# Kernel optimization log

Hardware: AMD Instinct MI355X
Metric: run time of the kernel (lower is better)

## Reference

```python
import jax, jax.numpy as jnp
from jax import lax
import numpy as np

BS, T, DA, DZ, K = 64, 512, 16, 32, 3


def _lstm_layer(x, Wih, Whh, bih, bhh):
    # x: [B, T, in], PyTorch LSTM gate order i,f,g,o; zero initial state
    B = x.shape[0]
    H = Whh.shape[1]
    b = bih + bhh

    def step(carry, xt):
        h, c = carry
        g = xt @ Wih.T + h @ Whh.T + b  # [B, 4H]
        i, f, gg, o = jnp.split(g, 4, axis=-1)
        c = jax.nn.sigmoid(f) * c + jax.nn.sigmoid(i) * jnp.tanh(gg)
        h = jax.nn.sigmoid(o) * jnp.tanh(c)
        return (h, c), h

    h0 = jnp.zeros((B, H), x.dtype)
    _, hs = lax.scan(step, (h0, h0), jnp.swapaxes(x, 0, 1))
    return jnp.swapaxes(hs, 0, 1)


def setup_inputs() -> dict:
    key = jax.random.key(0)
    ks = jax.random.split(key, 12)
    a = jax.random.normal(ks[0], (BS, T, DA), jnp.float32)
    # mixture dynamics / emission matrices, kept near identity for stability
    A = 0.95 * jnp.eye(DZ, dtype=jnp.float32) + 0.02 * jax.random.normal(ks[1], (K, T, DZ, DZ), jnp.float32)
    C = jnp.eye(DA, DZ, dtype=jnp.float32) + 0.05 * jax.random.normal(ks[2], (K, T, DA, DZ), jnp.float32)
    R = 0.1 * jnp.eye(DA, dtype=jnp.float32)
    Q = 0.1 * jnp.eye(DZ, dtype=jnp.float32)
    mu0 = jnp.zeros((DZ,), jnp.float32)
    sigma0 = jnp.eye(DZ, dtype=jnp.float32)
    H4 = 4 * K  # LSTM hidden size = K
    Wih0 = 0.1 * jax.random.normal(ks[3], (H4, DA), jnp.float32)
    Whh0 = 0.1 * jax.random.normal(ks[4], (H4, K), jnp.float32)
    bih0 = 0.1 * jax.random.normal(ks[5], (H4,), jnp.float32)
    bhh0 = 0.1 * jax.random.normal(ks[6], (H4,), jnp.float32)
    Wih1 = 0.1 * jax.random.normal(ks[7], (H4, K), jnp.float32)
    Whh1 = 0.1 * jax.random.normal(ks[8], (H4, K), jnp.float32)
    bih1 = 0.1 * jax.random.normal(ks[9], (H4,), jnp.float32)
    bhh1 = 0.1 * jax.random.normal(ks[10], (H4,), jnp.float32)
    return {"a": a, "A": A, "C": C, "R": R, "Q": Q, "mu0": mu0, "sigma0": sigma0,
            "Wih0": Wih0, "Whh0": Whh0, "bih0": bih0, "bhh0": bhh0,
            "Wih1": Wih1, "Whh1": Whh1, "bih1": bih1, "bhh1": bhh1}


def reference(a, A, C, R, Q, mu0, sigma0, Wih0, Whh0, bih0, bhh0, Wih1, Whh1, bih1, bhh1):
    bs, T, da = a.shape
    dz = A.shape[-1]
    # dynamics network: 2-layer LSTM + softmax mixture weights alpha [bs,T,K]
    h = _lstm_layer(a, Wih0, Whh0, bih0, bhh0)
    h = _lstm_layer(h, Wih1, Whh1, bih1, bhh1)
    alpha = jax.nn.softmax(h, axis=-1)
    # mix per-mode matrices; time-major [T,bs,.,.]
    At = jnp.einsum('btk,ktij->tbij', alpha, A)
    Ct = jnp.einsum('btk,ktij->tbij', alpha, C)
    a_tm = jnp.swapaxes(a, 0, 1)  # [T,bs,da]
    I = jnp.eye(dz, dtype=a.dtype)
    mu_f0 = jnp.broadcast_to(mu0, (bs, dz))
    sig_f0 = jnp.broadcast_to(sigma0, (bs, dz, dz))

    def fstep(carry, inp):
        mu_f, mu_p, sig_p = carry  # prev filtered mean, predicted mean/cov
        a_t, A_t, C_t = inp
        # NOTE: residual uses previous *filtered* mean, matching the source code
        r = a_t - jnp.einsum('bij,bj->bi', C_t, mu_f)
        Ct_T = jnp.swapaxes(C_t, -1, -2)
        S = C_t @ sig_p @ Ct_T + R
        Kg = sig_p @ Ct_T @ jnp.linalg.inv(S)
        mu_new = mu_p + jnp.einsum('bij,bj->bi', Kg, r)
        sig_new = (I - Kg @ C_t) @ sig_p
        mu_p_new = jnp.einsum('bij,bj->bi', A_t, mu_new)
        sig_p_new = A_t @ sig_new @ jnp.swapaxes(A_t, -1, -2) + Q
        return (mu_new, mu_p_new, sig_p_new), (mu_new, sig_new, mu_p_new, sig_p_new)

    _, (mu_f, sig_f, mu_p, sig_p) = lax.scan(
        fstep, (mu_f0, mu_f0, sig_f0), (a_tm, At, Ct))

    # RTS smoothing (backward recursion), faithful to smooth()
    def sstep(carry, inp):
        mu_n, sig_n = carry
        mu_ft, sig_ft, mu_pt, sig_pt, A_next = inp
        J = sig_ft @ jnp.swapaxes(A_next, -1, -2) @ jnp.linalg.inv(sig_pt)
        mu_s = mu_ft + jnp.einsum('bij,bj->bi', J, mu_n - mu_pt)
        sig_s = sig_ft + J @ (sig_n - sig_pt)
        return (mu_s, sig_s), (mu_s, sig_s)

    _, (mu_s_rest, sig_s_rest) = lax.scan(
        sstep, (mu_f[-1], sig_f[-1]),
        (mu_f[:-1], sig_f[:-1], mu_p[:-1], sig_p[:-1], At[1:]),
        reverse=True)
    mu_s = jnp.concatenate([mu_s_rest, mu_f[-1:]], axis=0)   # [T,bs,dz]
    sig_s = jnp.concatenate([sig_s_rest, sig_f[-1:]], axis=0)  # [T,bs,dz,dz]
    out = jnp.concatenate([mu_s, sig_s.reshape(T, bs, dz * dz)], axis=-1)
    return jnp.swapaxes(out, 0, 1)  # [bs, T, dz + dz*dz]
```

## Files before the change

kernel.cpp:

```cpp
#include <hip/hip_runtime.h>
#include <hip/hip_bf16.h>

#define BSZ 64
#define TT  512
#define DA  16
#define DZ  32
#define NG  12
#define NT  256

typedef __hip_bfloat16 bf;

#define FP32_R0 0x3DCCCCCDu

__device__ __forceinline__ int mode_(const void* Rm){
  return (((const unsigned*)Rm)[0] == FP32_R0) ? 0 : 1;
}
__device__ __forceinline__ float LD(const void* p, size_t i, int b16){
  return b16 ? __bfloat162float(((const bf*)p)[i]) : ((const float*)p)[i];
}
__device__ __forceinline__ void STO(void* p, size_t i, float v, int b16){
  if (b16) ((bf*)p)[i] = __float2bfloat16(v);
  else     ((float*)p)[i] = v;
}
__device__ __forceinline__ float osan_(double vd, float code){
  float v = (float)vd;
  unsigned u = __float_as_uint(v);
  if ((u & 0x7f800000u) == 0x7f800000u)
    return ((u & 0x007fffffu) != 0u) ? code : ((u >> 31) ? -(code-1000.0f) : (code-1000.0f));
  return v;
}
__device__ __forceinline__ float sigm_(float x){ return 1.0f/(1.0f + __expf(-x)); }
__device__ __forceinline__ float tanh_(float x){ return 1.0f - 2.0f/(__expf(2.0f*x)+1.0f); }

__device__ void alpha_stage_(int b, int tid, int b16,
  const void* a, const void* Wih0, const void* bih0, const void* bhh0,
  const void* Whh0, const void* Wih1, const void* Whh1,
  const void* bih1, const void* bhh1,
  float* sxw, float* salp)
{
  for (int e=tid; e<TT*NG; e+=NT){
    int t=e/NG, g=e-NG*t;
    float s = LD(bih0,g,b16) + LD(bhh0,g,b16);
    size_t ab = ((size_t)b*TT + t)*DA;
    #pragma unroll
    for (int j=0;j<DA;++j) s += LD(Wih0,g*DA+j,b16)*LD(a,ab+j,b16);
    sxw[e] = s;
  }
  __syncthreads();
  if (tid==0){
    float w0[NG][3], wi1[NG][3], w1[NG][3], bb[NG];
    #pragma unroll
    for (int g=0;g<NG;++g){
      #pragma unroll
      for (int j=0;j<3;++j){ w0[g][j]=LD(Whh0,(size_t)g*3+j,b16); wi1[g][j]=LD(Wih1,(size_t)g*3+j,b16); w1[g][j]=LD(Whh1,(size_t)g*3+j,b16); }
      bb[g] = LD(bih1,g,b16) + LD(bhh1,g,b16);
    }
    float h1[3]={0,0,0}, c1[3]={0,0,0}, h2[3]={0,0,0}, c2[3]={0,0,0};
    for (int t=0;t<TT;++t){
      const float* xr = sxw + t*NG;
      float g1[NG];
      #pragma unroll
      for (int g=0;g<NG;++g) g1[g] = xr[g] + w0[g][0]*h1[0]+w0[g][1]*h1[1]+w0[g][2]*h1[2];
      #pragma unroll
      for (int j=0;j<3;++j){
        float iv=sigm_(g1[j]), fv=sigm_(g1[3+j]), gv=tanh_(g1[6+j]), ov=sigm_(g1[9+j]);
        c1[j] = fv*c1[j] + iv*gv;
        h1[j] = ov*tanh_(c1[j]);
      }
      float g2[NG];
      #pragma unroll
      for (int g=0;g<NG;++g) g2[g] = bb[g] + wi1[g][0]*h1[0]+wi1[g][1]*h1[1]+wi1[g][2]*h1[2]
                                            + w1[g][0]*h2[0]+w1[g][1]*h2[1]+w1[g][2]*h2[2];
      #pragma unroll
      for (int j=0;j<3;++j){
        float iv=sigm_(g2[j]), fv=sigm_(g2[3+j]), gv=tanh_(g2[6+j]), ov=sigm_(g2[9+j]);
        c2[j] = fv*c2[j] + iv*gv;
        h2[j] = ov*tanh_(c2[j]);
      }
      float m = fmaxf(h2[0], fmaxf(h2[1], h2[2]));
      float e0=__expf(h2[0]-m), e1=__expf(h2[1]-m), e2=__expf(h2[2]-m);
      float inv = 1.0f/(e0+e1+e2);
      salp[t*3+0]=e0*inv; salp[t*3+1]=e1*inv; salp[t*3+2]=e2*inv;
    }
  }
  __syncthreads();
}

__global__ __launch_bounds__(256) void k_alpha(
  const void* __restrict__ a, const void* __restrict__ Rm,
  const void* __restrict__ Wih0, const void* __restrict__ Whh0,
  const void* __restrict__ bih0, const void* __restrict__ bhh0,
  const void* __restrict__ Wih1, const void* __restrict__ Whh1,
  const void* __restrict__ bih1, const void* __restrict__ bhh1,
  float* __restrict__ alws)
{
  const int b16 = mode_(Rm);
  const int b = blockIdx.x, tid = threadIdx.x;
  __shared__ float sxw[TT*NG];
  __shared__ float salp[TT*3];
  alpha_stage_(b, tid, b16, a, Wih0, bih0, bhh0, Whh0, Wih1, Whh1, bih1, bhh1,
               sxw, salp);
  for (int e=tid;e<TT*3;e+=NT) alws[(size_t)b*TT*3+e] = salp[e];
}

__global__ __launch_bounds__(256) void k_fwd(
  const void* __restrict__ a, const void* __restrict__ Am,
  const void* __restrict__ Cm, const void* __restrict__ Rm,
  const void* __restrict__ Qm, const void* __restrict__ mu0,
  const void* __restrict__ sig0,
  const void* __restrict__ Wih0, const void* __restrict__ Whh0,
  const void* __restrict__ bih0, const void* __restrict__ bhh0,
  const void* __restrict__ Wih1, const void* __restrict__ Whh1,
  const void* __restrict__ bih1, const void* __restrict__ bhh1,
  const float* __restrict__ alws,
  void* __restrict__ out)
{
  const int b16 = mode_(Rm);
  const int b = blockIdx.x, tid = threadIdx.x;
  __shared__ double dpool[4240];
  __shared__ float sAt[1056], sCt[528], sQ[1056], sR[272], sPCt[544], sKg[544];
  __shared__ float salp[TT*3];
  __shared__ double dMu[32], dMup[32], dr[16];
  double* dPp  = dpool;
  double* dPf  = dpool+1056;
  double* dCP  = dpool+2112;
  double* dT1  = dpool+2640;
  double* dAugS= dpool+3696;
  double* dMinv= dpool+3968;

  if (alws){
    for (int e=tid;e<TT*3;e+=NT) salp[e] = alws[(size_t)b*TT*3+e];
    __syncthreads();
  } else {
    alpha_stage_(b, tid, b16, a, Wih0, bih0, bhh0, Whh0, Wih1, Whh1, bih1, bhh1,
                 (float*)dpool, salp);
  }

  for (int e=tid;e<1024;e+=NT){ int i=e>>5,j=e&31;
    sQ[i*33+j]  = LD(Qm,e,b16);
    dPp[i*33+j] = (double)LD(sig0,e,b16); }
  for (int e=tid;e<256;e+=NT){ int i=e>>4,j=e&15; sR[i*17+j] = LD(Rm,e,b16); }
  if (tid<32){ double m = (double)LD(mu0,tid,b16); dMu[tid]=m; dMup[tid]=m; }
  __syncthreads();

  const int i0 = tid>>5, j0 = tid&31;
  const int i4 = tid>>4, j4 = tid&15;

  float pA0[4],pA1[4],pA2[4],pC0[2],pC1[2],pC2[2];
  {
    size_t o0=0, o1=(size_t)TT*1024, o2=(size_t)2*TT*1024;
    #pragma unroll
    for (int q=0;q<4;++q){ int e=tid+q*NT; pA0[q]=LD(Am,o0+e,b16); pA1[q]=LD(Am,o1+e,b16); pA2[q]=LD(Am,o2+e,b16); }
    size_t c0=0, c1=(size_t)TT*512, c2=(size_t)2*TT*512;
    #pragma unroll
    for (int q=0;q<2;++q){ int e=tid+q*NT; pC0[q]=LD(Cm,c0+e,b16); pC1[q]=LD(Cm,c1+e,b16); pC2[q]=LD(Cm,c2+e,b16); }
  }

  for (int t=0;t<TT;++t){
    const size_t ob = ((size_t)b*TT+t)*1056;
    {
      float a0=salp[t*3+0], a1=salp[t*3+1], a2=salp[t*3+2];
      #pragma unroll
      for (int q=0;q<4;++q){ int e=tid+q*NT; int i=e>>5,j=e&31;
        sAt[i*33+j] = a0*pA0[q]+a1*pA1[q]+a2*pA2[q]; }
      #pragma unroll
      for (int q=0;q<2;++q){ int e=tid+q*NT; int i=e>>5,j=e&31;
        sCt[i*33+j] = a0*pC0[q]+a1*pC1[q]+a2*pC2[q]; }
    }
    if (t+1<TT){
      size_t o0=(size_t)(t+1)*1024, o1=(size_t)(TT+t+1)*1024, o2=(size_t)(2*TT+t+1)*1024;
      #pragma unroll
      for (int q=0;q<4;++q){ int e=tid+q*NT; pA0[q]=LD(Am,o0+e,b16); pA1[q]=LD(Am,o1+e,b16); pA2[q]=LD(Am,o2+e,b16); }
      size_t c0=(size_t)(t+1)*512, c1=(size_t)(TT+t+1)*512, c2=(size_t)(2*TT+t+1)*512;
      #pragma unroll
      for (int q=0;q<2;++q){ int e=tid+q*NT; pC0[q]=LD(Cm,c0+e,b16); pC1[q]=LD(Cm,c1+e,b16); pC2[q]=LD(Cm,c2+e,b16); }
    }
    __syncthreads();

    {
      double A0=0.0, A1=0.0;
      for (int k=0;k<32;++k){ double bv=dPp[k*33+j0];
        A0 += (double)sCt[i0*33+k]*bv;
        A1 += (double)sCt[(i0+8)*33+k]*bv; }
      dCP[i0*33+j0]=A0; dCP[(i0+8)*33+j0]=A1;
    }
    {
      double A0=0.0, A1=0.0;
      for (int m=0;m<32;++m){ double cv=(double)sCt[j4*33+m];
        A0 += dPp[i4*33+m]*cv;
        A1 += dPp[(i4+16)*33+m]*cv; }
      sPCt[i4*17+j4]=(float)A0; sPCt[(i4+16)*17+j4]=(float)A1;
    }
    if (tid<16){ double s = (double)LD(a,((size_t)b*TT+t)*DA+tid,b16);
      for (int k=0;k<32;++k) s -= (double)sCt[tid*33+k]*dMu[k];
      dr[tid]=s; }
    __syncthreads();

    { int i=tid>>4, j=tid&15; double v=(double)sR[i*17+j];
      for (int k=0;k<32;++k) v += dCP[i*33+k]*(double)sCt[j*33+k];
      dAugS[i*17+j]=v; }
    __syncthreads();

    if (tid < 64){
      const int r = tid>>2, q = tid&3, cbase = q*8;
      double Rg[8];
      #pragma unroll
      for (int u=0;u<8;++u){
        int c = cbase+u;
        Rg[u] = (c<16) ? dAugS[r*17+c] : ((c-16)==r ? 1.0 : 0.0);
      }
      #pragma unroll
      for (int kp=0;kp<16;++kp){
        double pv = __shfl(Rg[kp&7], (kp<<2)|(kp>>3), 64);
        if (!(fabs(pv)>1e-300)) pv=1.0;
        double ip = 1.0/pv;
        if (r==kp){
          #pragma unroll
          for (int u=0;u<8;++u){ int c=cbase+u; if (c>kp) Rg[u]*=ip; }
        }
        double rf = __shfl(Rg[kp&7], (tid&0x3C)|(kp>>3), 64);
        #pragma unroll
        for (int u=0;u<8;++u){
          double pr = __shfl(Rg[u], (kp<<2)|q, 64);
          int c=cbase+u;
          if (r!=kp && c>kp) Rg[u] -= rf*pr;
        }
      }
      if (q>=2){
        #pragma unroll
        for (int u=0;u<8;++u){ int k=cbase+u-16; dMinv[r*17+k]=Rg[u]; }
      }
    }
    __syncthreads();

    {
      double A0=0.0, A1=0.0;
      for (int l=0;l<16;++l){ double mv=dMinv[l*17+j4];
        A0 += (double)sPCt[i4*17+l]*mv;
        A1 += (double)sPCt[(i4+16)*17+l]*mv; }
      sKg[i4*17+j4]=(float)A0; sKg[(i4+16)*17+j4]=(float)A1;
    }
    __syncthreads();

    if (tid<32){ double s=dMup[tid];
      for (int k=0;k<16;++k) s += (double)sKg[tid*17+k]*dr[k];
      dMu[tid]=s;
      STO(out, ob+tid, osan_(s,5300.0f), b16);
    }
    {
      double A0=dPp[i0*33+j0], A1=dPp[(i0+8)*33+j0],
             A2=dPp[(i0+16)*33+j0], A3=dPp[(i0+24)*33+j0];
      for (int l=0;l<16;++l){ double cv=dCP[l*33+j0];
        A0 -= (double)sKg[i0*17+l]*cv;
        A1 -= (double)sKg[(i0+8)*17+l]*cv;
        A2 -= (double)sKg[(i0+16)*17+l]*cv;
        A3 -= (double)sKg[(i0+24)*17+l]*cv; }
      dPf[i0*33+j0]=A0; dPf[(i0+8)*33+j0]=A1;
      dPf[(i0+16)*33+j0]=A2; dPf[(i0+24)*33+j0]=A3;
      STO(out, ob+32+((size_t)i0<<5)+j0,      osan_(A0,5300.0f), b16);
      STO(out, ob+32+((size_t)(i0+8)<<5)+j0,  osan_(A1,5300.0f), b16);
      STO(out, ob+32+((size_t)(i0+16)<<5)+j0, osan_(A2,5300.0f), b16);
      STO(out, ob+32+((size_t)(i0+24)<<5)+j0, osan_(A3,5300.0f), b16);
    }
    __syncthreads();

    {
      double A0=0.0,A1=0.0,A2=0.0,A3=0.0;
      for (int k=0;k<32;++k){ double bv=dPf[k*33+j0];
        A0 += (double)sAt[i0*33+k]*bv;
        A1 += (double)sAt[(i0+8)*33+k]*bv;
        A2 += (double)sAt[(i0+16)*33+k]*bv;
        A3 += (double)sAt[(i0+24)*33+k]*bv; }
      dT1[i0*33+j0]=A0; dT1[(i0+8)*33+j0]=A1;
      dT1[(i0+16)*33+j0]=A2; dT1[(i0+24)*33+j0]=A3;
    }
    if (tid<32){ double s=0.0;
      for (int k=0;k<32;++k) s += (double)sAt[tid*33+k]*dMu[k];
      dMup[tid]=s; }
    __syncthreads();

    {
      double A0=(double)sQ[i0*33+j0], A1=(double)sQ[(i0+8)*33+j0],
             A2=(double)sQ[(i0+16)*33+j0], A3=(double)sQ[(i0+24)*33+j0];
      for (int k=0;k<32;++k){ double av=(double)sAt[j0*33+k];
        A0 += dT1[i0*33+k]*av;
        A1 += dT1[(i0+8)*33+k]*av;
        A2 += dT1[(i0+16)*33+k]*av;
        A3 += dT1[(i0+24)*33+k]*av; }
      dPp[i0*33+j0]=A0; dPp[(i0+8)*33+j0]=A1;
      dPp[(i0+16)*33+j0]=A2; dPp[(i0+24)*33+j0]=A3;
    }
    __syncthreads();
  }
}

__global__ __launch_bounds__(256) void k_pre(
  const void* __restrict__ Am, const void* __restrict__ Qm,
  const void* __restrict__ Rm, const void* __restrict__ outv,
  const float* __restrict__ alws, float* __restrict__ rec, int t0)
{
  const int b16 = mode_(Rm);
  const int t = t0 + blockIdx.x;
  const int b = blockIdx.y;
  const int tid = threadIdx.x;
  __shared__ double dAug[2080];
  __shared__ double dmp[32];
  __shared__ float sAtc[1056], sAtn[1056], sSf[1056], sT[1056], sF[1056], sPp[1056], sJ[1056], sQ[1056];
  __shared__ float smu[32];

  size_t obase = (size_t)b*TT*1056;
  const float* al = alws + (size_t)b*TT*3;
  float c0=al[t*3+0],     c1=al[t*3+1],     c2=al[t*3+2];
  float n0=al[(t+1)*3+0], n1=al[(t+1)*3+1], n2=al[(t+1)*3+2];
  size_t oA0c=(size_t)t*1024, oA1c=(size_t)(TT+t)*1024, oA2c=(size_t)(2*TT+t)*1024;
  size_t oA0n=oA0c+1024, oA1n=oA1c+1024, oA2n=oA2c+1024;

  for (int e=tid;e<1024;e+=NT){ int i=e>>5,j=e&31;
    sAtc[i*33+j] = c0*LD(Am,oA0c+e,b16)+c1*LD(Am,oA1c+e,b16)+c2*LD(Am,oA2c+e,b16);
    sAtn[i*33+j] = n0*LD(Am,oA0n+e,b16)+n1*LD(Am,oA1n+e,b16)+n2*LD(Am,oA2n+e,b16);
    sSf[i*33+j]  = LD(outv, obase + (size_t)t*1056 + 32 + e, b16);
    sQ[i*33+j]   = LD(Qm,e,b16);
  }
  if (tid<32) smu[tid] = LD(outv, obase + (size_t)t*1056 + tid, b16);
  __syncthreads();

  for (int e=tid;e<1024;e+=NT){ int i=e>>5, j=e&31;
    double acc=0.0, accF=0.0;
    for (int k=0;k<32;++k){
      acc  += (double)sAtc[i*33+k]*(double)sSf[k*33+j];
      accF += (double)sSf[i*33+k]*(double)sAtn[j*33+k];
    }
    sT[i*33+j]=(float)acc; sF[i*33+j]=(float)accF; }
  if (tid<32){ double s=0.0;
    for (int k=0;k<32;++k) s += (double)sAtc[tid*33+k]*(double)smu[k];
    dmp[tid]=s; }
  __syncthreads();

  for (int e=tid;e<1024;e+=NT){ int i=e>>5, j=e&31;
    double acc=(double)sQ[i*33+j];
    for (int k=0;k<32;++k) acc += (double)sT[i*33+k]*(double)sAtc[j*33+k];
    sPp[i*33+j]=(float)acc;
    dAug[i*65+j]=acc;
    dAug[i*65+32+j]=(i==j)?1.0:0.0; }
  __syncthreads();

  for (int kp=0;kp<32;++kp){
    double pv = dAug[kp*65+kp];
    if (!(fabs(pv)>1e-300)) pv=1.0;
    double ip = 1.0/pv;
    if (tid<64 && tid>kp) dAug[kp*65+tid] *= ip;
    __syncthreads();
    for (int e=tid;e<2048;e+=NT){ int i=e>>6, j=e&63;
      if (i!=kp && j>kp) dAug[i*65+j] -= dAug[i*65+kp]*dAug[kp*65+j];
    }
    __syncthreads();
  }

  float* rp = rec + ((size_t)b*gridDim.x + (size_t)blockIdx.x)*2080;

  for (int e=tid;e<1024;e+=NT){ int i=e>>5, j=e&31; double acc=0.0;
    for (int k=0;k<32;++k) acc += (double)sF[i*33+k]*dAug[k*65+32+j];
    float jv=(float)acc; sJ[i*33+j]=jv; rp[e]=jv; }
  __syncthreads();

  for (int e=tid;e<1024;e+=NT){ int i=e>>5, j=e&31;
    double acc=(double)sSf[i*33+j];
    for (int k=0;k<32;++k) acc -= (double)sJ[i*33+k]*(double)sPp[k*33+j];
    rp[1024+e]=(float)acc; }
  if (tid<32){ double acc=(double)smu[tid];
    for (int k=0;k<32;++k) acc -= (double)sJ[tid*33+k]*dmp[k];
    rp[2048+tid]=(float)acc; }
}

__global__ __launch_bounds__(256) void k_bwd(
  const void* __restrict__ Rm, void* __restrict__ outv,
  const float* __restrict__ rec, float* __restrict__ cont,
  int t0, int t1)
{
  const int b16 = mode_(Rm);
  const int b = blockIdx.x, tid = threadIdx.x;
  const int chlen = t1 - t0;
  __shared__ float sX[2][1056];
  __shared__ float sR[2080];
  size_t obase = (size_t)b*TT*1056;
  int cur = 0;
  const int i0 = tid>>5, j0 = tid&31;

  if (t1 == TT-1){
    for (int e=tid;e<1024;e+=NT){ int i=e>>5,j=e&31;
      sX[0][i*33+j] = LD(outv, obase+(size_t)(TT-1)*1056+32+e, b16); }
    if (tid<32) sX[0][tid*33+32] = LD(outv, obase+(size_t)(TT-1)*1056+tid, b16);
  } else {
    for (int e=tid;e<1056;e+=NT) sX[0][e] = cont[(size_t)b*1056+e];
  }
  float rg[9];
  {
    const float* rp = rec + ((size_t)b*chlen + (size_t)(chlen-1))*2080;
    #pragma unroll
    for (int q=0;q<9;++q){ int e=tid+q*NT; rg[q] = (e<2080)? rp[e] : 0.0f; }
  }
  __syncthreads();

  for (int t=t1-1; t>=t0; --t){
    #pragma unroll
    for (int q=0;q<9;++q){ int e=tid+q*NT; if (e<2080) sR[e]=rg[q]; }
    if (t>t0){
      const float* rp = rec + ((size_t)b*chlen + (size_t)(t-1-t0))*2080;
      #pragma unroll
      for (int q=0;q<9;++q){ int e=tid+q*NT; rg[q] = (e<2080)? rp[e] : 0.0f; }
    }
    __syncthreads();

    const float* Xc = sX[cur]; float* Xn = sX[cur^1];
    {
      double A0=(double)sR[1024+(i0<<5)+j0];
      double A1=(double)sR[1024+((i0+8)<<5)+j0];
      double A2=(double)sR[1024+((i0+16)<<5)+j0];
      double A3=(double)sR[1024+((i0+24)<<5)+j0];
      for (int k=0;k<32;++k){ double xv=(double)Xc[k*33+j0];
        A0 += (double)sR[(i0<<5)+k]*xv;
        A1 += (double)sR[((i0+8)<<5)+k]*xv;
        A2 += (double)sR[((i0+16)<<5)+k]*xv;
        A3 += (double)sR[((i0+24)<<5)+k]*xv; }
      Xn[i0*33+j0]=(float)A0;      Xn[(i0+8)*33+j0]=(float)A1;
      Xn[(i0+16)*33+j0]=(float)A2; Xn[(i0+24)*33+j0]=(float)A3;
      size_t tb = obase+(size_t)t*1056+32;
      STO(outv, tb+((size_t)i0<<5)+j0,      osan_(A0,5700.0f), b16);
      STO(outv, tb+((size_t)(i0+8)<<5)+j0,  osan_(A1,5700.0f), b16);
      STO(outv, tb+((size_t)(i0+16)<<5)+j0, osan_(A2,5700.0f), b16);
      STO(outv, tb+((size_t)(i0+24)<<5)+j0, osan_(A3,5700.0f), b16);
    }
    if (tid<32){
      double acc=(double)sR[2048+tid];
      for (int k=0;k<32;++k) acc += (double)sR[(tid<<5)+k]*(double)Xc[k*33+32];
      Xn[tid*33+32]=(float)acc;
      STO(outv, obase+(size_t)t*1056+tid, osan_(acc,5700.0f), b16);
    }
    __syncthreads();
    cur ^= 1;
  }
  for (int e=tid;e<1056;e+=NT) cont[(size_t)b*1056+e] = sX[cur][e];
}

__global__ __launch_bounds__(256) void k_smooth(
  const void* __restrict__ a, const void* __restrict__ Am,
  const void* __restrict__ Rm, const void* __restrict__ Qm,
  const void* __restrict__ Wih0, const void* __restrict__ Whh0,
  const void* __restrict__ bih0, const void* __restrict__ bhh0,
  const void* __restrict__ Wih1, const void* __restrict__ Whh1,
  const void* __restrict__ bih1, const void* __restrict__ bhh1,
  void* __restrict__ out)
{
  const int b16 = mode_(Rm);
  const int b = blockIdx.x, tid = threadIdx.x;
  __shared__ double dAug[2080];
  __shared__ float fp2[9504];
  __shared__ float salp[TT*3];
  __shared__ double dMun[32], dmp[32], sdm[32];
  float* sAtn = fp2;
  float* sAtc = fp2+1056;
  float* sSf  = fp2+2112;
  float* sSn  = fp2+3168;
  float* sT   = fp2+4224;
  float* sQ   = fp2+5280;
  float* sF   = fp2+6336;
  float* sPp32= fp2+7392;
  float* sJ   = fp2+8448;

  alpha_stage_(b, tid, b16, a, Wih0, bih0, bhh0, Whh0, Wih1, Whh1, bih1, bhh1,
               fp2, salp);

  size_t obase = (size_t)b*TT*1056;
  for (int e=tid;e<1024;e+=NT){ int i=e>>5,j=e&31;
    sQ[i*33+j]  = LD(Qm,e,b16);
    sSn[i*33+j] = LD(out, obase + (size_t)(TT-1)*1056 + 32 + e, b16); }
  if (tid<32) dMun[tid] = (double)LD(out, obase + (size_t)(TT-1)*1056 + tid, b16);
  __syncthreads();

  for (int t=TT-2; t>=0; --t){
    float n0=salp[(t+1)*3+0], n1=salp[(t+1)*3+1], n2=salp[(t+1)*3+2];
    float c0=salp[t*3+0],     c1=salp[t*3+1],     c2=salp[t*3+2];
    size_t oA0n=(size_t)(t+1)*1024, oA1n=(size_t)(TT+t+1)*1024, oA2n=(size_t)(2*TT+t+1)*1024;
    size_t oA0c=(size_t)t*1024,     oA1c=(size_t)(TT+t)*1024,   oA2c=(size_t)(2*TT+t)*1024;
    for (int e=tid;e<1024;e+=NT){ int i=e>>5,j=e&31;
      sAtn[i*33+j] = n0*LD(Am,oA0n+e,b16)+n1*LD(Am,oA1n+e,b16)+n2*LD(Am,oA2n+e,b16);
      sAtc[i*33+j] = c0*LD(Am,oA0c+e,b16)+c1*LD(Am,oA1c+e,b16)+c2*LD(Am,oA2c+e,b16);
      sSf[i*33+j]  = LD(out, obase + (size_t)t*1056 + 32 + e, b16); }
    __syncthreads();

    for (int e=tid;e<1024;e+=NT){ int i=e>>5, j=e&31;
      double acc=0.0, accF=0.0;
      for (int k=0;k<32;++k){
        acc  += (double)sAtc[i*33+k]*(double)sSf[k*33+j];
        accF += (double)sSf[i*33+k]*(double)sAtn[j*33+k];
      }
      sT[i*33+j]=(float)acc; sF[i*33+j]=(float)accF; }
    if (tid<32){ double s=0.0; float muf = LD(out, obase+(size_t)t*1056+tid, b16);
      for (int k=0;k<32;++k) s += (double)sAtc[tid*33+k]*(double)LD(out, obase+(size_t)t*1056+k, b16);
      dmp[tid]=s; (void)muf; }
    __syncthreads();

    for (int e=tid;e<1024;e+=NT){ int i=e>>5, j=e&31;
      double acc=(double)sQ[i*33+j];
      for (int k=0;k<32;++k) acc += (double)sT[i*33+k]*(double)sAtc[j*33+k];
      sPp32[i*33+j]=(float)acc;
      dAug[i*65+j]=acc;
      dAug[i*65+32+j]=(i==j)?1.0:0.0; }
    if (tid<32) sdm[tid] = dMun[tid] - dmp[tid];
    __syncthreads();

    for (int kp=0;kp<32;++kp){
      double pv = dAug[kp*65+kp];
      if (!(fabs(pv)>1e-300)) pv=1.0;
      double ip = 1.0/pv;
      if (tid<64 && tid>kp) dAug[kp*65+tid] *= ip;
      __syncthreads();
      for (int e=tid;e<2048;e+=NT){ int i=e>>6, j=e&63;
        if (i!=kp && j>kp) dAug[i*65+j] -= dAug[i*65+kp]*dAug[kp*65+j];
      }
      __syncthreads();
    }

    for (int e=tid;e<1024;e+=NT){ int i=e>>5, j=e&31; double acc=0.0;
      for (int k=0;k<32;++k) acc += (double)sF[i*33+k]*dAug[k*65+32+j];
      sJ[i*33+j]=(float)acc; }
    __syncthreads();

    if (tid<32){ double s2=0.0;
      for (int k=0;k<32;++k) s2 += (double)sJ[tid*33+k]*sdm[k];
      double v = (double)LD(out, obase+(size_t)t*1056+tid, b16) + s2;
      STO(out, obase+(size_t)t*1056+tid, osan_(v,5700.0f), b16);
      dMun[tid] = v;
    }
    float resv[4];
    { int i0 = tid>>5, j = tid&31;
      for (int s=0;s<4;++s){ int i=i0+(s<<3); double acc=0.0;
        for (int k=0;k<32;++k) acc += (double)sJ[i*33+k]*((double)sSn[k*33+j]-(double)sPp32[k*33+j]);
        double res = (double)sSf[i*33+j] + acc;
        STO(out, obase+(size_t)t*1056+32+(i<<5)+j, osan_(res,5700.0f), b16);
        resv[s]=(float)res;
      }
    }
    __syncthreads();
    { int i0 = tid>>5, j = tid&31;
      for (int s=0;s<4;++s){ int i=i0+(s<<3); sSn[i*33+j]=resv[s]; } }
    __syncthreads();
  }
}

__global__ __launch_bounds__(256) void k_fill(float* o, int n, float v){
  int i = blockIdx.x*256 + threadIdx.x;
  if (i<n) o[i]=v;
}

extern "C" void kernel_launch(void* const* d_in, const int* in_sizes, int n_in,
                              void* d_out, int out_size, void* d_ws, size_t ws_size,
                              hipStream_t stream)
{
  static const int EXP[15] = {524288,1572864,786432,256,1024,32,1024,192,36,12,12,36,36,12,12};
  int ok = (n_in==15) && (out_size==34603008);
  if (ok) for (int i=0;i<15;++i) if (in_sizes[i]!=EXP[i]) ok=0;
  if (!ok){
    k_fill<<<dim3((out_size+255)/256), dim3(256), 0, stream>>>((float*)d_out, out_size, 777.0f);
    return;
  }
  const void* a=d_in[0]; const void* Am=d_in[1]; const void* Cm=d_in[2];
  const void* Rm=d_in[3]; const void* Qm=d_in[4]; const void* mu0=d_in[5];
  const void* sig0=d_in[6];
  const void* Wih0=d_in[7]; const void* Whh0=d_in[8]; const void* bih0=d_in[9];
  const void* bhh0=d_in[10]; const void* Wih1=d_in[11]; const void* Whh1=d_in[12];
  const void* bih1=d_in[13]; const void* bhh1=d_in[14];

  const long long FIXED_F = 98304LL + 67584LL;
  long long availB = (long long)ws_size;
  int CH = 0;
  if (d_ws && availB > FIXED_F*4){
    long long ch = (availB - FIXED_F*4) / (64LL*2080LL*4LL);
    CH = (int)((ch > 511) ? 511 : ch);
  }

  if (CH >= 4){
    float* wsf  = (float*)d_ws;
    float* alws = wsf;
    float* cont = wsf + 98304;
    float* rec  = wsf + 165888;

    k_alpha<<<dim3(BSZ), dim3(NT), 0, stream>>>(a, Rm,
        Wih0, Whh0, bih0, bhh0, Wih1, Whh1, bih1, bhh1, alws);
    k_fwd  <<<dim3(BSZ), dim3(NT), 0, stream>>>(a, Am, Cm, Rm, Qm, mu0, sig0,
        Wih0, Whh0, bih0, bhh0, Wih1, Whh1, bih1, bhh1, alws, d_out);

    int t1 = TT-1;
    while (t1 > 0){
      int t0 = t1 - CH; if (t0 < 0) t0 = 0;
      int len = t1 - t0;
      k_pre<<<dim3(len, BSZ), dim3(NT), 0, stream>>>(Am, Qm, Rm, d_out, alws, rec, t0);
      k_bwd<<<dim3(BSZ), dim3(NT), 0, stream>>>(Rm, d_out, rec, cont, t0, t1);
      t1 = t0;
    }
  } else {
    k_fwd   <<<dim3(BSZ), dim3(NT), 0, stream>>>(a, Am, Cm, Rm, Qm, mu0, sig0,
               Wih0, Whh0, bih0, bhh0, Wih1, Whh1, bih1, bhh1, (const float*)nullptr, d_out);
    k_smooth<<<dim3(BSZ), dim3(NT), 0, stream>>>(a, Am, Rm, Qm,
               Wih0, Whh0, bih0, bhh0, Wih1, Whh1, bih1, bhh1, d_out);
  }
}
```

Before: 10.67 ms.

## Cache forward predicted covariances in workspace for the smoother precompute

The forward filter now writes each step's predicted mean and covariance to workspace. The smoother precompute kernel reads them back instead of recomputing A_t·Σ·A_tᵀ+Q and A_t·μ, which removes two 32x32 double matmuls per timestep. The cost is a 128MB workspace buffer and extra global writes in the serial forward kernel, plus smaller chunks for the backward pass if workspace is tight. Many inner loops also get unroll pragmas, and one Xc column is hoisted into registers in the backward kernel.

```diff
diff --git a/kernel.cpp b/kernel.cpp
--- a/kernel.cpp
+++ b/kernel.cpp
@@ -32,13 +32,13 @@
 __device__ __forceinline__ float sigm_(float x){ return 1.0f/(1.0f + __expf(-x)); }
 __device__ __forceinline__ float tanh_(float x){ return 1.0f - 2.0f/(__expf(2.0f*x)+1.0f); }
 
-__device__ void alpha_stage_(int b, int tid, int b16,
+__device__ void alpha_stage_(int b, int tid, int nt, int b16,
   const void* a, const void* Wih0, const void* bih0, const void* bhh0,
   const void* Whh0, const void* Wih1, const void* Whh1,
   const void* bih1, const void* bhh1,
   float* sxw, float* salp)
 {
-  for (int e=tid; e<TT*NG; e+=NT){
+  for (int e=tid; e<TT*NG; e+=nt){
     int t=e/NG, g=e-NG*t;
     float s = LD(bih0,g,b16) + LD(bhh0,g,b16);
     size_t ab = ((size_t)b*TT + t)*DA;
@@ -98,7 +98,7 @@
   const int b = blockIdx.x, tid = threadIdx.x;
   __shared__ float sxw[TT*NG];
   __shared__ float salp[TT*3];
-  alpha_stage_(b, tid, b16, a, Wih0, bih0, bhh0, Whh0, Wih1, Whh1, bih1, bhh1,
+  alpha_stage_(b, tid, NT, b16, a, Wih0, bih0, bhh0, Whh0, Wih1, Whh1, bih1, bhh1,
                sxw, salp);
   for (int e=tid;e<TT*3;e+=NT) alws[(size_t)b*TT*3+e] = salp[e];
 }
@@ -113,6 +113,7 @@
   const void* __restrict__ Wih1, const void* __restrict__ Whh1,
   const void* __restrict__ bih1, const void* __restrict__ bhh1,
   const float* __restrict__ alws,
+  float* __restrict__ psig, float* __restrict__ pmu,
   void* __restrict__ out)
 {
   const int b16 = mode_(Rm);
@@ -132,7 +133,7 @@
     for (int e=tid;e<TT*3;e+=NT) salp[e] = alws[(size_t)b*TT*3+e];
     __syncthreads();
   } else {
-    alpha_stage_(b, tid, b16, a, Wih0, bih0, bhh0, Whh0, Wih1, Whh1, bih1, bhh1,
+    alpha_stage_(b, tid, NT, b16, a, Wih0, bih0, bhh0, Whh0, Wih1, Whh1, bih1, bhh1,
                  (float*)dpool, salp);
   }
 
@@ -276,7 +277,9 @@
     }
     if (tid<32){ double s=0.0;
       for (int k=0;k<32;++k) s += (double)sAt[tid*33+k]*dMu[k];
-      dMup[tid]=s; }
+      dMup[tid]=s;
+      if (pmu) pmu[((size_t)b*TT+t)*32+tid] = (float)s;
+    }
     __syncthreads();
 
     {
@@ -289,6 +292,13 @@
         A3 += dT1[(i0+24)*33+k]*av; }
       dPp[i0*33+j0]=A0; dPp[(i0+8)*33+j0]=A1;
       dPp[(i0+16)*33+j0]=A2; dPp[(i0+24)*33+j0]=A3;
+      if (psig){
+        size_t pb = ((size_t)b*TT+t)*1024;
+        psig[pb+((size_t)i0<<5)+j0]      = (float)A0;
+        psig[pb+((size_t)(i0+8)<<5)+j0]  = (float)A1;
+        psig[pb+((size_t)(i0+16)<<5)+j0] = (float)A2;
+        psig[pb+((size_t)(i0+24)<<5)+j0] = (float)A3;
+      }
     }
     __syncthreads();
   }
@@ -297,7 +307,9 @@
 __global__ __launch_bounds__(256) void k_pre(
   const void* __restrict__ Am, const void* __restrict__ Qm,
   const void* __restrict__ Rm, const void* __restrict__ outv,
-  const float* __restrict__ alws, float* __restrict__ rec, int t0)
+  const float* __restrict__ alws,
+  const float* __restrict__ psig, const float* __restrict__ pmu,
+  float* __restrict__ rec, int t0)
 {
   const int b16 = mode_(Rm);
   const int t = t0 + blockIdx.x;
@@ -310,39 +322,67 @@
 
   size_t obase = (size_t)b*TT*1056;
   const float* al = alws + (size_t)b*TT*3;
-  float c0=al[t*3+0],     c1=al[t*3+1],     c2=al[t*3+2];
   float n0=al[(t+1)*3+0], n1=al[(t+1)*3+1], n2=al[(t+1)*3+2];
-  size_t oA0c=(size_t)t*1024, oA1c=(size_t)(TT+t)*1024, oA2c=(size_t)(2*TT+t)*1024;
-  size_t oA0n=oA0c+1024, oA1n=oA1c+1024, oA2n=oA2c+1024;
-
-  for (int e=tid;e<1024;e+=NT){ int i=e>>5,j=e&31;
-    sAtc[i*33+j] = c0*LD(Am,oA0c+e,b16)+c1*LD(Am,oA1c+e,b16)+c2*LD(Am,oA2c+e,b16);
-    sAtn[i*33+j] = n0*LD(Am,oA0n+e,b16)+n1*LD(Am,oA1n+e,b16)+n2*LD(Am,oA2n+e,b16);
-    sSf[i*33+j]  = LD(outv, obase + (size_t)t*1056 + 32 + e, b16);
-    sQ[i*33+j]   = LD(Qm,e,b16);
-  }
-  if (tid<32) smu[tid] = LD(outv, obase + (size_t)t*1056 + tid, b16);
-  __syncthreads();
-
-  for (int e=tid;e<1024;e+=NT){ int i=e>>5, j=e&31;
-    double acc=0.0, accF=0.0;
-    for (int k=0;k<32;++k){
-      acc  += (double)sAtc[i*33+k]*(double)sSf[k*33+j];
-      accF += (double)sSf[i*33+k]*(double)sAtn[j*33+k];
-    }
-    sT[i*33+j]=(float)acc; sF[i*33+j]=(float)accF; }
-  if (tid<32){ double s=0.0;
-    for (int k=0;k<32;++k) s += (double)sAtc[tid*33+k]*(double)smu[k];
-    dmp[tid]=s; }
-  __syncthreads();
-
-  for (int e=tid;e<1024;e+=NT){ int i=e>>5, j=e&31;
-    double acc=(double)sQ[i*33+j];
-    for (int k=0;k<32;++k) acc += (double)sT[i*33+k]*(double)sAtc[j*33+k];
-    sPp[i*33+j]=(float)acc;
-    dAug[i*65+j]=acc;
-    dAug[i*65+32+j]=(i==j)?1.0:0.0; }
-  __syncthreads();
+  size_t oA0n=(size_t)(t+1)*1024, oA1n=(size_t)(TT+t+1)*1024, oA2n=(size_t)(2*TT+t+1)*1024;
+
+  if (psig){
+    const float* pb = psig + ((size_t)b*TT+t)*1024;
+    for (int e=tid;e<1024;e+=NT){ int i=e>>5,j=e&31;
+      sAtn[i*33+j] = n0*LD(Am,oA0n+e,b16)+n1*LD(Am,oA1n+e,b16)+n2*LD(Am,oA2n+e,b16);
+      sSf[i*33+j]  = LD(outv, obase + (size_t)t*1056 + 32 + e, b16);
+      float sp = pb[e];
+      sPp[i*33+j] = sp;
+      dAug[i*65+j] = (double)sp;
+      dAug[i*65+32+j] = (i==j)?1.0:0.0;
+    }
+    if (tid<32){
+      smu[tid] = LD(outv, obase + (size_t)t*1056 + tid, b16);
+      dmp[tid] = (double)pmu[((size_t)b*TT+t)*32+tid];
+    }
+    __syncthreads();
+
+    for (int e=tid;e<1024;e+=NT){ int i=e>>5, j=e&31;
+      double accF=0.0;
+      #pragma unroll
+      for (int k=0;k<32;++k) accF += (double)sSf[i*33+k]*(double)sAtn[j*33+k];
+      sF[i*33+j]=(float)accF; }
+    __syncthreads();
+  } else {
+    float c0=al[t*3+0], c1=al[t*3+1], c2=al[t*3+2];
+    size_t oA0c=(size_t)t*1024, oA1c=(size_t)(TT+t)*1024, oA2c=(size_t)(2*TT+t)*1024;
+
+    for (int e=tid;e<1024;e+=NT){ int i=e>>5,j=e&31;
+      sAtc[i*33+j] = c0*LD(Am,oA0c+e,b16)+c1*LD(Am,oA1c+e,b16)+c2*LD(Am,oA2c+e,b16);
+      sAtn[i*33+j] = n0*LD(Am,oA0n+e,b16)+n1*LD(Am,oA1n+e,b16)+n2*LD(Am,oA2n+e,b16);
+      sSf[i*33+j]  = LD(outv, obase + (size_t)t*1056 + 32 + e, b16);
+      sQ[i*33+j]   = LD(Qm,e,b16);
+    }
+    if (tid<32) smu[tid] = LD(outv, obase + (size_t)t*1056 + tid, b16);
+    __syncthreads();
+
+    for (int e=tid;e<1024;e+=NT){ int i=e>>5, j=e&31;
+      double acc=0.0, accF=0.0;
+      #pragma unroll
+      for (int k=0;k<32;++k){
+        acc  += (double)sAtc[i*33+k]*(double)sSf[k*33+j];
+        accF += (double)sSf[i*33+k]*(double)sAtn[j*33+k];
+      }
+      sT[i*33+j]=(float)acc; sF[i*33+j]=(float)accF; }
+    if (tid<32){ double s=0.0;
+      #pragma unroll
+      for (int k=0;k<32;++k) s += (double)sAtc[tid*33+k]*(double)smu[k];
+      dmp[tid]=s; }
+    __syncthreads();
+
+    for (int e=tid;e<1024;e+=NT){ int i=e>>5, j=e&31;
+      double acc=(double)sQ[i*33+j];
+      #pragma unroll
+      for (int k=0;k<32;++k) acc += (double)sT[i*33+k]*(double)sAtc[j*33+k];
+      sPp[i*33+j]=(float)acc;
+      dAug[i*65+j]=acc;
+      dAug[i*65+32+j]=(i==j)?1.0:0.0; }
+    __syncthreads();
+  }
 
   for (int kp=0;kp<32;++kp){
     double pv = dAug[kp*65+kp];
@@ -350,7 +390,8 @@
     double ip = 1.0/pv;
     if (tid<64 && tid>kp) dAug[kp*65+tid] *= ip;
     __syncthreads();
-    for (int e=tid;e<2048;e+=NT){ int i=e>>6, j=e&63;
+    #pragma unroll
+    for (int q=0;q<8;++q){ int e=tid+q*NT; int i=e>>6, j=e&63;
       if (i!=kp && j>kp) dAug[i*65+j] -= dAug[i*65+kp]*dAug[kp*65+j];
     }
     __syncthreads();
@@ -359,15 +400,18 @@
   float* rp = rec + ((size_t)b*gridDim.x + (size_t)blockIdx.x)*2080;
 
   for (int e=tid;e<1024;e+=NT){ int i=e>>5, j=e&31; double acc=0.0;
+    #pragma unroll
     for (int k=0;k<32;++k) acc += (double)sF[i*33+k]*dAug[k*65+32+j];
     float jv=(float)acc; sJ[i*33+j]=jv; rp[e]=jv; }
   __syncthreads();
 
   for (int e=tid;e<1024;e+=NT){ int i=e>>5, j=e&31;
     double acc=(double)sSf[i*33+j];
+    #pragma unroll
     for (int k=0;k<32;++k) acc -= (double)sJ[i*33+k]*(double)sPp[k*33+j];
     rp[1024+e]=(float)acc; }
   if (tid<32){ double acc=(double)smu[tid];
+    #pragma unroll
     for (int k=0;k<32;++k) acc -= (double)sJ[tid*33+k]*dmp[k];
     rp[2048+tid]=(float)acc; }
 }
@@ -413,11 +457,15 @@
 
     const float* Xc = sX[cur]; float* Xn = sX[cur^1];
     {
+      float colX[32];
+      #pragma unroll
+      for (int k=0;k<32;++k) colX[k] = Xc[k*33+j0];
       double A0=(double)sR[1024+(i0<<5)+j0];
       double A1=(double)sR[1024+((i0+8)<<5)+j0];
       double A2=(double)sR[1024+((i0+16)<<5)+j0];
       double A3=(double)sR[1024+((i0+24)<<5)+j0];
-      for (int k=0;k<32;++k){ double xv=(double)Xc[k*33+j0];
+      #pragma unroll
+      for (int k=0;k<32;++k){ double xv=(double)colX[k];
         A0 += (double)sR[(i0<<5)+k]*xv;
         A1 += (double)sR[((i0+8)<<5)+k]*xv;
         A2 += (double)sR[((i0+16)<<5)+k]*xv;
@@ -432,6 +480,7 @@
     }
     if (tid<32){
       double acc=(double)sR[2048+tid];
+      #pragma unroll
       for (int k=0;k<32;++k) acc += (double)sR[(tid<<5)+k]*(double)Xc[k*33+32];
       Xn[tid*33+32]=(float)acc;
       STO(outv, obase+(size_t)t*1056+tid, osan_(acc,5700.0f), b16);
@@ -467,7 +516,7 @@
   float* sPp32= fp2+7392;
   float* sJ   = fp2+8448;
 
-  alpha_stage_(b, tid, b16, a, Wih0, bih0, bhh0, Whh0, Wih1, Whh1, bih1, bhh1,
+  alpha_stage_(b, tid, NT, b16, a, Wih0, bih0, bhh0, Whh0, Wih1, Whh1, bih1, bhh1,
                fp2, salp);
 
   size_t obase = (size_t)b*TT*1056;
@@ -490,18 +539,21 @@
 
     for (int e=tid;e<1024;e+=NT){ int i=e>>5, j=e&31;
       double acc=0.0, accF=0.0;
+      #pragma unroll
       for (int k=0;k<32;++k){
         acc  += (double)sAtc[i*33+k]*(double)sSf[k*33+j];
         accF += (double)sSf[i*33+k]*(double)sAtn[j*33+k];
       }
       sT[i*33+j]=(float)acc; sF[i*33+j]=(float)accF; }
     if (tid<32){ double s=0.0; float muf = LD(out, obase+(size_t)t*1056+tid, b16);
+      #pragma unroll
       for (int k=0;k<32;++k) s += (double)sAtc[tid*33+k]*(double)LD(out, obase+(size_t)t*1056+k, b16);
       dmp[tid]=s; (void)muf; }
     __syncthreads();
 
     for (int e=tid;e<1024;e+=NT){ int i=e>>5, j=e&31;
       double acc=(double)sQ[i*33+j];
+      #pragma unroll
       for (int k=0;k<32;++k) acc += (double)sT[i*33+k]*(double)sAtc[j*33+k];
       sPp32[i*33+j]=(float)acc;
       dAug[i*65+j]=acc;
@@ -522,11 +574,13 @@
     }
 
     for (int e=tid;e<1024;e+=NT){ int i=e>>5, j=e&31; double acc=0.0;
+      #pragma unroll
       for (int k=0;k<32;++k) acc += (double)sF[i*33+k]*dAug[k*65+32+j];
       sJ[i*33+j]=(float)acc; }
     __syncthreads();
 
     if (tid<32){ double s2=0.0;
+      #pragma unroll
       for (int k=0;k<32;++k) s2 += (double)sJ[tid*33+k]*sdm[k];
       double v = (double)LD(out, obase+(size_t)t*1056+tid, b16) + s2;
       STO(out, obase+(size_t)t*1056+tid, osan_(v,5700.0f), b16);
@@ -535,6 +589,7 @@
     float resv[4];
     { int i0 = tid>>5, j = tid&31;
       for (int s=0;s<4;++s){ int i=i0+(s<<3); double acc=0.0;
+        #pragma unroll
         for (int k=0;k<32;++k) acc += (double)sJ[i*33+k]*((double)sSn[k*33+j]-(double)sPp32[k*33+j]);
         double res = (double)sSf[i*33+j] + acc;
         STO(out, obase+(size_t)t*1056+32+(i<<5)+j, osan_(res,5700.0f), b16);
@@ -571,36 +626,47 @@
   const void* bhh0=d_in[10]; const void* Wih1=d_in[11]; const void* Whh1=d_in[12];
   const void* bih1=d_in[13]; const void* bhh1=d_in[14];
 
-  const long long FIXED_F = 98304LL + 67584LL;
-  long long availB = (long long)ws_size;
-  int CH = 0;
-  if (d_ws && availB > FIXED_F*4){
-    long long ch = (availB - FIXED_F*4) / (64LL*2080LL*4LL);
-    CH = (int)((ch > 511) ? 511 : ch);
+  const long long ALF = 98304LL, CONTF = 67584LL;
+  const long long PMUF = 64LL*512*32, PSIGF = 64LL*512*1024;
+  long long availF = (long long)(ws_size/4);
+  int CH = 0, use_psig = 0;
+  if (d_ws){
+    long long remF = availF - (ALF+CONTF+PMUF+PSIGF);
+    long long ch = remF / (64LL*2080LL);
+    if (ch >= 4){ use_psig = 1; CH = (int)((ch>511)?511:ch); }
+    else {
+      remF = availF - (ALF+CONTF);
+      ch = remF / (64LL*2080LL);
+      if (ch >= 4) CH = (int)((ch>511)?511:ch);
+    }
   }
 
   if (CH >= 4){
     float* wsf  = (float*)d_ws;
     float* alws = wsf;
-    float* cont = wsf + 98304;
-    float* rec  = wsf + 165888;
+    float* cont = wsf + ALF;
+    float* pmu  = use_psig ? (wsf + ALF + CONTF) : nullptr;
+    float* psig = use_psig ? (pmu + PMUF) : nullptr;
+    float* rec  = use_psig ? (psig + PSIGF) : (wsf + ALF + CONTF);
 
     k_alpha<<<dim3(BSZ), dim3(NT), 0, stream>>>(a, Rm,
         Wih0, Whh0, bih0, bhh0, Wih1, Whh1, bih1, bhh1, alws);
     k_fwd  <<<dim3(BSZ), dim3(NT), 0, stream>>>(a, Am, Cm, Rm, Qm, mu0, sig0,
-        Wih0, Whh0, bih0, bhh0, Wih1, Whh1, bih1, bhh1, alws, d_out);
+        Wih0, Whh0, bih0, bhh0, Wih1, Whh1, bih1, bhh1, alws, psig, pmu, d_out);
 
     int t1 = TT-1;
     while (t1 > 0){
       int t0 = t1 - CH; if (t0 < 0) t0 = 0;
       int len = t1 - t0;
-      k_pre<<<dim3(len, BSZ), dim3(NT), 0, stream>>>(Am, Qm, Rm, d_out, alws, rec, t0);
+      k_pre<<<dim3(len, BSZ), dim3(NT), 0, stream>>>(Am, Qm, Rm, d_out, alws,
+          psig, pmu, rec, t0);
       k_bwd<<<dim3(BSZ), dim3(NT), 0, stream>>>(Rm, d_out, rec, cont, t0, t1);
       t1 = t0;
     }
   } else {
     k_fwd   <<<dim3(BSZ), dim3(NT), 0, stream>>>(a, Am, Cm, Rm, Qm, mu0, sig0,
-               Wih0, Whh0, bih0, bhh0, Wih1, Whh1, bih1, bhh1, (const float*)nullptr, d_out);
+               Wih0, Whh0, bih0, bhh0, Wih1, Whh1, bih1, bhh1,
+               (const float*)nullptr, (float*)nullptr, (float*)nullptr, d_out);
     k_smooth<<<dim3(BSZ), dim3(NT), 0, stream>>>(a, Am, Rm, Qm,
                Wih0, Whh0, bih0, bhh0, Wih1, Whh1, bih1, bhh1, d_out);
   }
```

Measured after the change: 10.05 ms. 1.06x faster.
